# Kernel tuning notes

Measured on AMD Instinct MI355X. Metric: run time of the kernel, lower is better.

Reference implementation:

```python
import math
import jax, jax.numpy as jnp
import numpy as np

B, L, S, H, E, D = 2, 2048, 2048, 8, 64, 64


def setup_inputs() -> dict:
    key = jax.random.key(0)
    kq, kk, kv = jax.random.split(key, 3)
    return {
        "queries": jax.random.normal(kq, (B, L, H, E), dtype=jnp.float32),
        "keys": jax.random.normal(kk, (B, S, H, E), dtype=jnp.float32),
        "values": jax.random.normal(kv, (B, S, H, D), dtype=jnp.float32),
    }


def reference(queries, keys, values):
    b, l, h, e = queries.shape
    s = keys.shape[1]
    # source truncates queries if L > S
    if l > s:
        queries = queries[:, :s]
        l = s
    # dense scores [B,H,L,S]
    scores = jnp.einsum('blhe,bshe->bhls', queries, keys)
    # sparsity measure per query: max - mean over keys
    M_sp = scores.max(axis=-1) - scores.sum(axis=-1) / s  # [B,H,L]
    # k = min(max(L*log(S),1), L); for S>=3 this equals L (all queries, reordered)
    k = min(int(max(l * math.log(s), 1)), l)
    _, top_k = jax.lax.top_k(M_sp, k)  # [B,H,k], descending by M_sp
    # gather selected query rows of the score matrix
    topk_scores = jnp.take_along_axis(scores, top_k[..., None], axis=2)  # [B,H,k,S]
    topk_scores = topk_scores - topk_scores.max(axis=-1, keepdims=True)
    A = jax.nn.softmax(topk_scores / math.sqrt(e), axis=-1)  # [B,H,k,S]
    # attend (output in top-k-permuted query order, as in source)
    V = jnp.einsum('bhls,bshd->blhd', A, values)  # [B,k,H,D]
    return V
```

## Files before the change

### kernel.cpp

```cpp
#include <hip/hip_runtime.h>
#include <math.h>

#define BB 2
#define LL 2048
#define SS 2048
#define HH 8
#define EE 64
#define DD 64
#define HE (HH * EE)


typedef __attribute__((ext_vector_type(8))) short   bf16x8;
typedef __attribute__((ext_vector_type(4))) float   f32x4;
typedef __attribute__((ext_vector_type(8))) unsigned short u16x8;
typedef __attribute__((ext_vector_type(4))) unsigned short u16x4;

__device__ __forceinline__ unsigned short f2bf(float x) {
    unsigned int u = __float_as_uint(x);
    return (unsigned short)((u + 0x7FFFu + ((u >> 16) & 1u)) >> 16);
}

__device__ __forceinline__ float rdlane(float v, int lane) {
    return __uint_as_float(
        (unsigned)__builtin_amdgcn_readlane((int)__float_as_uint(v), lane));
}

__global__ __launch_bounds__(256, 2)
void msp_partial(const float* __restrict__ Q, const float* __restrict__ K,
                 float* __restrict__ pscratch) {
#pragma clang fp contract(off)
    const int bid = blockIdx.x;
    const int hf = bid >> 9;
    const int rem = bid & 511;
    const int lt = rem & 31, bh = rem >> 5;
    const int h = bh & 7, b = bh >> 3;
    const int t = threadIdx.x, lq = t & 63, w = t >> 6;
    const int l = lt * 64 + lq;

    float qf[64];
    const float4* qrow = (const float4*)(Q + (((size_t)b * LL + l) * HH + h) * EE);
#pragma unroll
    for (int i = 0; i < 16; i++) {
        float4 v = qrow[i];
        qf[4*i] = v.x; qf[4*i+1] = v.y; qf[4*i+2] = v.z; qf[4*i+3] = v.w;
    }

    const float* Kw = K + (((size_t)b * SS) * HH + h) * EE
                        + (size_t)(hf * 512 + w * 128) * HE;
    const float* gld = Kw + (size_t)(lq >> 4) * HE + (lq & 15) * 4;

    float4 A0 = *(const float4*)(gld);
    float4 B0 = *(const float4*)(gld + 4 * HE);

    float mx = -1e30f;
    float r[8];
#pragma unroll 1
    for (int i8 = 0; i8 < 16; ++i8) {
        const int kc = i8 * 8;
        const int kn = (kc < 120) ? kc + 8 : 120;

        float4 A1 = *(const float4*)(gld + (size_t)kn * HE);
        float4 B1 = *(const float4*)(gld + (size_t)(kn + 4) * HE);

        float c[8];
#pragma unroll
        for (int j = 0; j < 8; ++j) c[j] = 0.f;
#pragma unroll
        for (int j = 0; j < 4; ++j) {
#pragma unroll
            for (int e4 = 0; e4 < 16; ++e4) {
                const int ln = j * 16 + e4;
                c[j] = fmaf(qf[4*e4+0], rdlane(A0.x, ln), c[j]);
                c[j] = fmaf(qf[4*e4+1], rdlane(A0.y, ln), c[j]);
                c[j] = fmaf(qf[4*e4+2], rdlane(A0.z, ln), c[j]);
                c[j] = fmaf(qf[4*e4+3], rdlane(A0.w, ln), c[j]);
            }
        }
#pragma unroll
        for (int j = 0; j < 4; ++j) {
#pragma unroll
            for (int e4 = 0; e4 < 16; ++e4) {
                const int ln = j * 16 + e4;
                c[4+j] = fmaf(qf[4*e4+0], rdlane(B0.x, ln), c[4+j]);
                c[4+j] = fmaf(qf[4*e4+1], rdlane(B0.y, ln), c[4+j]);
                c[4+j] = fmaf(qf[4*e4+2], rdlane(B0.z, ln), c[4+j]);
                c[4+j] = fmaf(qf[4*e4+3], rdlane(B0.w, ln), c[4+j]);
            }
        }
#pragma unroll
        for (int j = 0; j < 8; ++j) {
            mx = fmaxf(mx, c[j]);
            if (i8 == 0) r[j] = c[j];
            else         r[j] = __fadd_rn(r[j], c[j]);
        }
        A0 = A1; B0 = B1;
    }
    const float blkv = __fadd_rn(
        __fadd_rn(__fadd_rn(r[0], r[1]), __fadd_rn(r[2], r[3])),
        __fadd_rn(__fadd_rn(r[4], r[5]), __fadd_rn(r[6], r[7])));

    __shared__ float smx[4][64], sblk[4][64];
    smx[w][lq] = mx; sblk[w][lq] = blkv;
    __syncthreads();
    if (w == 0) {
        const float m_all = fmaxf(fmaxf(smx[0][lq], smx[1][lq]),
                                  fmaxf(smx[2][lq], smx[3][lq]));
        const float sub = __fadd_rn(
            __fadd_rn(sblk[0][lq], sblk[1][lq]),
            __fadd_rn(sblk[2][lq], sblk[3][lq]));
        pscratch[(((size_t)hf * 16 + bh) << 11) + l]          = m_all;
        pscratch[131072 + (((size_t)hf * 16 + bh) << 11) + l] = sub;
    }
}

__global__ __launch_bounds__(1024)
void sort_rank(const float* __restrict__ pscratch, float* __restrict__ maxs,
               int* __restrict__ rank) {
    __shared__ unsigned int k1[2048];
    __shared__ int pay[2048];
    const int bh = blockIdx.x;
    const int t = threadIdx.x;
    for (int i = t; i < 2048; i += 1024) {
        const float p0 = pscratch[(((size_t)(0 * 16 + bh)) << 11) + i];
        const float p1 = pscratch[(((size_t)(1 * 16 + bh)) << 11) + i];
        const float p2 = pscratch[(((size_t)(2 * 16 + bh)) << 11) + i];
        const float p3 = pscratch[(((size_t)(3 * 16 + bh)) << 11) + i];
        const float s0 = pscratch[131072 + (((size_t)(0 * 16 + bh)) << 11) + i];
        const float s1 = pscratch[131072 + (((size_t)(1 * 16 + bh)) << 11) + i];
        const float s2 = pscratch[131072 + (((size_t)(2 * 16 + bh)) << 11) + i];
        const float s3 = pscratch[131072 + (((size_t)(3 * 16 + bh)) << 11) + i];
        const float m_all = fmaxf(fmaxf(p0, p1), fmaxf(p2, p3));
        const float s2048 = __fadd_rn(__fadd_rn(s0, s1), __fadd_rn(s2, s3));
        const float mean  = __fmul_rn(s2048, 0.00048828125f);
        const float msp   = __fsub_rn(m_all, mean);
        maxs[(((size_t)bh) << 11) + i] = m_all;
        unsigned int u = __float_as_uint(msp);
        u = (u & 0x80000000u) ? ~u : (u | 0x80000000u);
        k1[i] = u; pay[i] = i;
    }
    __syncthreads();
    for (int k = 2; k <= 2048; k <<= 1) {
        for (int j = k >> 1; j > 0; j >>= 1) {
            for (int i = t; i < 2048; i += 1024) {
                const int ixj = i ^ j;
                if (ixj > i) {
                    unsigned int a1 = k1[i], c1 = k1[ixj];
                    int pa = pay[i], pc = pay[ixj];
                    const bool pre = (a1 > c1) || (a1 == c1 && pa < pc);
                    const bool dir = ((i & k) == 0);
                    if (dir != pre) {
                        k1[i] = c1; k1[ixj] = a1;
                        pay[i] = pc; pay[ixj] = pa;
                    }
                }
            }
            __syncthreads();
        }
    }
    for (int i = t; i < 2048; i += 1024)
        rank[(((size_t)bh) << 11) + pay[i]] = i;
}

__global__ __launch_bounds__(256, 2)
void flash_mfma(const float* __restrict__ Q, const float* __restrict__ K,
                const float* __restrict__ V, const float* __restrict__ maxs,
                const int* __restrict__ rank, float* __restrict__ out) {
    __shared__ unsigned short ldsK[2][64 * 72];
    __shared__ unsigned short ldsVT[2][64 * 72];
    __shared__ unsigned short ldsP[4 * 16 * 72];

    const int bid = blockIdx.x;
    const int bh = bid & 15, lt = bid >> 4;
    const int h = bh & 7, b = bh >> 3;
    const int t = threadIdx.x, lane = t & 63, w = t >> 6;
    const int quad = lane >> 4, cl = lane & 15;

    const size_t kvbase = (((size_t)b * SS) * HH + h) * EE;

    bf16x8 qa[2];
    {
        const float* qp = Q + (((size_t)b * LL + (lt * 64 + w * 16 + cl)) * HH + h) * EE
                          + quad * 8;
#pragma unroll
        for (int ef = 0; ef < 2; ++ef) {
            float4 a0 = *(const float4*)(qp + ef * 32);
            float4 a1 = *(const float4*)(qp + ef * 32 + 4);
            short* s = (short*)&qa[ef];
            s[0] = (short)f2bf(a0.x); s[1] = (short)f2bf(a0.y);
            s[2] = (short)f2bf(a0.z); s[3] = (short)f2bf(a0.w);
            s[4] = (short)f2bf(a1.x); s[5] = (short)f2bf(a1.y);
            s[6] = (short)f2bf(a1.z); s[7] = (short)f2bf(a1.w);
        }
    }

    float negpm[4];
    int rk[4];
#pragma unroll
    for (int reg = 0; reg < 4; ++reg) {
        const int qg = lt * 64 + w * 16 + quad * 4 + reg;
        negpm[reg] = -0.125f * maxs[((size_t)bh << 11) + qg];
        rk[reg]    = rank[((size_t)bh << 11) + qg];
    }

    f32x4 accO[4];
#pragma unroll
    for (int nt = 0; nt < 4; ++nt) accO[nt] = (f32x4){0.f, 0.f, 0.f, 0.f};
    float ell[4] = {0.f, 0.f, 0.f, 0.f};

    const int pbase = w * (16 * 72);

    const int krow = t >> 2, kcol = (t & 3) * 16;
    const int vs0 = (t & 15) * 4, vd0 = (t >> 4) * 4;

    {
        const float* gp = K + kvbase + (size_t)krow * HE + kcol;
        float4 f0 = ((const float4*)gp)[0];
        float4 f1 = ((const float4*)gp)[1];
        float4 f2 = ((const float4*)gp)[2];
        float4 f3 = ((const float4*)gp)[3];
        const float* gv = V + kvbase + (size_t)vs0 * HE + vd0;
        float4 v0 = *(const float4*)(gv);
        float4 v1 = *(const float4*)(gv + HE);
        float4 v2 = *(const float4*)(gv + 2 * HE);
        float4 v3 = *(const float4*)(gv + 3 * HE);
        u16x8 w0 = { f2bf(f0.x), f2bf(f0.y), f2bf(f0.z), f2bf(f0.w),
                     f2bf(f1.x), f2bf(f1.y), f2bf(f1.z), f2bf(f1.w) };
        u16x8 w1 = { f2bf(f2.x), f2bf(f2.y), f2bf(f2.z), f2bf(f2.w),
                     f2bf(f3.x), f2bf(f3.y), f2bf(f3.z), f2bf(f3.w) };
        *(u16x8*)&ldsK[0][krow * 72 + kcol]     = w0;
        *(u16x8*)&ldsK[0][krow * 72 + kcol + 8] = w1;
        u16x4 p0 = { f2bf(v0.x), f2bf(v1.x), f2bf(v2.x), f2bf(v3.x) };
        u16x4 p1 = { f2bf(v0.y), f2bf(v1.y), f2bf(v2.y), f2bf(v3.y) };
        u16x4 p2 = { f2bf(v0.z), f2bf(v1.z), f2bf(v2.z), f2bf(v3.z) };
        u16x4 p3 = { f2bf(v0.w), f2bf(v1.w), f2bf(v2.w), f2bf(v3.w) };
        *(u16x4*)&ldsVT[0][(vd0 + 0) * 72 + vs0] = p0;
        *(u16x4*)&ldsVT[0][(vd0 + 1) * 72 + vs0] = p1;
        *(u16x4*)&ldsVT[0][(vd0 + 2) * 72 + vs0] = p2;
        *(u16x4*)&ldsVT[0][(vd0 + 3) * 72 + vs0] = p3;
    }
    __syncthreads();

    int cur = 0;
#pragma unroll 1
    for (int c0 = 0; c0 < SS; c0 += 64) {
        const bool more = (c0 + 64 < SS);
        float4 f0, f1, f2, f3, v0, v1, v2, v3;
        if (more) {
            const float* gp = K + kvbase + (size_t)(c0 + 64 + krow) * HE + kcol;
            f0 = ((const float4*)gp)[0];
            f1 = ((const float4*)gp)[1];
            f2 = ((const float4*)gp)[2];
            f3 = ((const float4*)gp)[3];
            const float* gv = V + kvbase + (size_t)(c0 + 64 + vs0) * HE + vd0;
            v0 = *(const float4*)(gv);
            v1 = *(const float4*)(gv + HE);
            v2 = *(const float4*)(gv + 2 * HE);
            v3 = *(const float4*)(gv + 3 * HE);
        }

        f32x4 Sc[4];
#pragma unroll
        for (int nt = 0; nt < 4; ++nt) {
            bf16x8 bk0 = *(const bf16x8*)&ldsK[cur][(nt * 16 + cl) * 72 + quad * 8];
            bf16x8 bk1 = *(const bf16x8*)&ldsK[cur][(nt * 16 + cl) * 72 + quad * 8 + 32];
            f32x4 z = (f32x4){0.f, 0.f, 0.f, 0.f};
            z = __builtin_amdgcn_mfma_f32_16x16x32_bf16(qa[0], bk0, z, 0, 0, 0);
            z = __builtin_amdgcn_mfma_f32_16x16x32_bf16(qa[1], bk1, z, 0, 0, 0);
            Sc[nt] = z;
        }

#pragma unroll
        for (int nt = 0; nt < 4; ++nt) {
#pragma unroll
            for (int reg = 0; reg < 4; ++reg) {
                const float p = __expf(fmaf(Sc[nt][reg], 0.125f, negpm[reg]));
                ell[reg] += p;
                ldsP[pbase + (quad * 4 + reg) * 72 + nt * 16 + cl] = f2bf(p);
            }
        }

        bf16x8 pa0 = *(const bf16x8*)&ldsP[pbase + cl * 72 + quad * 8];
        bf16x8 pa1 = *(const bf16x8*)&ldsP[pbase + cl * 72 + quad * 8 + 32];
#pragma unroll
        for (int nt = 0; nt < 4; ++nt) {
            bf16x8 bv0 = *(const bf16x8*)&ldsVT[cur][(nt * 16 + cl) * 72 + quad * 8];
            bf16x8 bv1 = *(const bf16x8*)&ldsVT[cur][(nt * 16 + cl) * 72 + quad * 8 + 32];
            accO[nt] = __builtin_amdgcn_mfma_f32_16x16x32_bf16(pa0, bv0, accO[nt], 0, 0, 0);
            accO[nt] = __builtin_amdgcn_mfma_f32_16x16x32_bf16(pa1, bv1, accO[nt], 0, 0, 0);
        }

        if (more) {
            u16x8 w0 = { f2bf(f0.x), f2bf(f0.y), f2bf(f0.z), f2bf(f0.w),
                         f2bf(f1.x), f2bf(f1.y), f2bf(f1.z), f2bf(f1.w) };
            u16x8 w1 = { f2bf(f2.x), f2bf(f2.y), f2bf(f2.z), f2bf(f2.w),
                         f2bf(f3.x), f2bf(f3.y), f2bf(f3.z), f2bf(f3.w) };
            *(u16x8*)&ldsK[cur ^ 1][krow * 72 + kcol]     = w0;
            *(u16x8*)&ldsK[cur ^ 1][krow * 72 + kcol + 8] = w1;
            u16x4 p0 = { f2bf(v0.x), f2bf(v1.x), f2bf(v2.x), f2bf(v3.x) };
            u16x4 p1 = { f2bf(v0.y), f2bf(v1.y), f2bf(v2.y), f2bf(v3.y) };
            u16x4 p2 = { f2bf(v0.z), f2bf(v1.z), f2bf(v2.z), f2bf(v3.z) };
            u16x4 p3 = { f2bf(v0.w), f2bf(v1.w), f2bf(v2.w), f2bf(v3.w) };
            *(u16x4*)&ldsVT[cur ^ 1][(vd0 + 0) * 72 + vs0] = p0;
            *(u16x4*)&ldsVT[cur ^ 1][(vd0 + 1) * 72 + vs0] = p1;
            *(u16x4*)&ldsVT[cur ^ 1][(vd0 + 2) * 72 + vs0] = p2;
            *(u16x4*)&ldsVT[cur ^ 1][(vd0 + 3) * 72 + vs0] = p3;
        }
        __syncthreads();
        cur ^= 1;
    }

#pragma unroll
    for (int reg = 0; reg < 4; ++reg) {
        float e = ell[reg];
        e += __shfl_xor(e, 1);
        e += __shfl_xor(e, 2);
        e += __shfl_xor(e, 4);
        e += __shfl_xor(e, 8);
        ell[reg] = 1.0f / e;
    }

#pragma unroll
    for (int reg = 0; reg < 4; ++reg) {
        float* orow = out + (((size_t)b * LL + rk[reg]) * HH + h) * DD;
#pragma unroll
        for (int nt = 0; nt < 4; ++nt)
            orow[nt * 16 + cl] = accO[nt][reg] * ell[reg];
    }
}

extern "C" void kernel_launch(void* const* d_in, const int* in_sizes, int n_in,
                              void* d_out, int out_size, void* d_ws, size_t ws_size,
                              hipStream_t stream) {
    const float* Q = (const float*)d_in[0];
    const float* K = (const float*)d_in[1];
    const float* V = (const float*)d_in[2];
    float* out = (float*)d_out;

    int*   rank = (int*)((char*)d_ws + 131072);
    float* maxs = (float*)((char*)d_ws + 262144);

    msp_partial<<<4 * BB * HH * (LL / 64), 256, 0, stream>>>(Q, K, out);
    sort_rank<<<BB * HH, 1024, 0, stream>>>(out, maxs, rank);
    flash_mfma<<<BB * HH * (LL / 64), 256, 0, stream>>>(Q, K, V, maxs, rank, out);
}
```

Measured before the change: 354.1 us.

## Give each wave private 16-key K/V tiles to drop block barriers

Each wave now loads and converts its own 16-key slice of K and V into private LDS buffers and walks the key dimension 16 at a time, which removes the block-wide __syncthreads from the main loop. The aim is to cut barrier stalls between waves. In exchange every wave re-reads all of K and V from global memory, four times the block's previous traffic. The PV MFMA now runs half-empty because lanes in quads 2-3 feed zeros, and the single-buffered tiles leave little room to hide load latency.

```diff
diff --git a/kernel.cpp b/kernel.cpp
--- a/kernel.cpp
+++ b/kernel.cpp
@@ -165,15 +165,16 @@
 void flash_mfma(const float* __restrict__ Q, const float* __restrict__ K,
                 const float* __restrict__ V, const float* __restrict__ maxs,
                 const int* __restrict__ rank, float* __restrict__ out) {
-    __shared__ unsigned short ldsK[2][64 * 72];
-    __shared__ unsigned short ldsVT[2][64 * 72];
-    __shared__ unsigned short ldsP[4 * 16 * 72];
+    __shared__ unsigned short ldsK[4][16 * 72];
+    __shared__ unsigned short ldsVT[4][64 * 24];
+    __shared__ unsigned short ldsP[4][16 * 72];
 
     const int bid = blockIdx.x;
     const int bh = bid & 15, lt = bid >> 4;
     const int h = bh & 7, b = bh >> 3;
     const int t = threadIdx.x, lane = t & 63, w = t >> 6;
     const int quad = lane >> 4, cl = lane & 15;
+    const int qq = quad & 1;
 
     const size_t kvbase = (((size_t)b * SS) * HH + h) * EE;
 
@@ -207,106 +208,93 @@
     for (int nt = 0; nt < 4; ++nt) accO[nt] = (f32x4){0.f, 0.f, 0.f, 0.f};
     float ell[4] = {0.f, 0.f, 0.f, 0.f};
 
-    const int pbase = w * (16 * 72);
-
-    const int krow = t >> 2, kcol = (t & 3) * 16;
-    const int vs0 = (t & 15) * 4, vd0 = (t >> 4) * 4;
+    unsigned short* Kw  = ldsK[w];
+    unsigned short* VTw = ldsVT[w];
+    unsigned short* Pw  = ldsP[w];
+
+    const int kr = lane >> 2, kc = (lane & 3) * 16;
+    const int vd = (lane >> 2) * 4, vs = (lane & 3) * 4;
+
+    float4 kf0, kf1, kf2, kf3, vf0, vf1, vf2, vf3;
 
     {
-        const float* gp = K + kvbase + (size_t)krow * HE + kcol;
-        float4 f0 = ((const float4*)gp)[0];
-        float4 f1 = ((const float4*)gp)[1];
-        float4 f2 = ((const float4*)gp)[2];
-        float4 f3 = ((const float4*)gp)[3];
-        const float* gv = V + kvbase + (size_t)vs0 * HE + vd0;
-        float4 v0 = *(const float4*)(gv);
-        float4 v1 = *(const float4*)(gv + HE);
-        float4 v2 = *(const float4*)(gv + 2 * HE);
-        float4 v3 = *(const float4*)(gv + 3 * HE);
-        u16x8 w0 = { f2bf(f0.x), f2bf(f0.y), f2bf(f0.z), f2bf(f0.w),
-                     f2bf(f1.x), f2bf(f1.y), f2bf(f1.z), f2bf(f1.w) };
-        u16x8 w1 = { f2bf(f2.x), f2bf(f2.y), f2bf(f2.z), f2bf(f2.w),
-                     f2bf(f3.x), f2bf(f3.y), f2bf(f3.z), f2bf(f3.w) };
-        *(u16x8*)&ldsK[0][krow * 72 + kcol]     = w0;
-        *(u16x8*)&ldsK[0][krow * 72 + kcol + 8] = w1;
-        u16x4 p0 = { f2bf(v0.x), f2bf(v1.x), f2bf(v2.x), f2bf(v3.x) };
-        u16x4 p1 = { f2bf(v0.y), f2bf(v1.y), f2bf(v2.y), f2bf(v3.y) };
-        u16x4 p2 = { f2bf(v0.z), f2bf(v1.z), f2bf(v2.z), f2bf(v3.z) };
-        u16x4 p3 = { f2bf(v0.w), f2bf(v1.w), f2bf(v2.w), f2bf(v3.w) };
-        *(u16x4*)&ldsVT[0][(vd0 + 0) * 72 + vs0] = p0;
-        *(u16x4*)&ldsVT[0][(vd0 + 1) * 72 + vs0] = p1;
-        *(u16x4*)&ldsVT[0][(vd0 + 2) * 72 + vs0] = p2;
-        *(u16x4*)&ldsVT[0][(vd0 + 3) * 72 + vs0] = p3;
-    }
-    __syncthreads();
-
-    int cur = 0;
+        const float* gp = K + kvbase + (size_t)kr * HE + kc;
+        kf0 = ((const float4*)gp)[0]; kf1 = ((const float4*)gp)[1];
+        kf2 = ((const float4*)gp)[2]; kf3 = ((const float4*)gp)[3];
+        const float* gv = V + kvbase + (size_t)vs * HE + vd;
+        vf0 = *(const float4*)(gv);
+        vf1 = *(const float4*)(gv + HE);
+        vf2 = *(const float4*)(gv + 2 * HE);
+        vf3 = *(const float4*)(gv + 3 * HE);
+        u16x8 a = { f2bf(kf0.x), f2bf(kf0.y), f2bf(kf0.z), f2bf(kf0.w),
+                    f2bf(kf1.x), f2bf(kf1.y), f2bf(kf1.z), f2bf(kf1.w) };
+        u16x8 b2 = { f2bf(kf2.x), f2bf(kf2.y), f2bf(kf2.z), f2bf(kf2.w),
+                     f2bf(kf3.x), f2bf(kf3.y), f2bf(kf3.z), f2bf(kf3.w) };
+        *(u16x8*)&Kw[kr * 72 + kc]     = a;
+        *(u16x8*)&Kw[kr * 72 + kc + 8] = b2;
+        u16x4 p0 = { f2bf(vf0.x), f2bf(vf1.x), f2bf(vf2.x), f2bf(vf3.x) };
+        u16x4 p1 = { f2bf(vf0.y), f2bf(vf1.y), f2bf(vf2.y), f2bf(vf3.y) };
+        u16x4 p2 = { f2bf(vf0.z), f2bf(vf1.z), f2bf(vf2.z), f2bf(vf3.z) };
+        u16x4 p3 = { f2bf(vf0.w), f2bf(vf1.w), f2bf(vf2.w), f2bf(vf3.w) };
+        *(u16x4*)&VTw[(vd + 0) * 24 + vs] = p0;
+        *(u16x4*)&VTw[(vd + 1) * 24 + vs] = p1;
+        *(u16x4*)&VTw[(vd + 2) * 24 + vs] = p2;
+        *(u16x4*)&VTw[(vd + 3) * 24 + vs] = p3;
+    }
+
+    const bf16x8 zero8 = (bf16x8){0, 0, 0, 0, 0, 0, 0, 0};
+
 #pragma unroll 1
-    for (int c0 = 0; c0 < SS; c0 += 64) {
-        const bool more = (c0 + 64 < SS);
-        float4 f0, f1, f2, f3, v0, v1, v2, v3;
+    for (int c0 = 0; c0 < SS; c0 += 16) {
+        const bool more = (c0 + 16 < SS);
         if (more) {
-            const float* gp = K + kvbase + (size_t)(c0 + 64 + krow) * HE + kcol;
-            f0 = ((const float4*)gp)[0];
-            f1 = ((const float4*)gp)[1];
-            f2 = ((const float4*)gp)[2];
-            f3 = ((const float4*)gp)[3];
-            const float* gv = V + kvbase + (size_t)(c0 + 64 + vs0) * HE + vd0;
-            v0 = *(const float4*)(gv);
-            v1 = *(const float4*)(gv + HE);
-            v2 = *(const float4*)(gv + 2 * HE);
-            v3 = *(const float4*)(gv + 3 * HE);
-        }
-
-        f32x4 Sc[4];
+            const float* gp = K + kvbase + (size_t)(c0 + 16 + kr) * HE + kc;
+            kf0 = ((const float4*)gp)[0]; kf1 = ((const float4*)gp)[1];
+            kf2 = ((const float4*)gp)[2]; kf3 = ((const float4*)gp)[3];
+            const float* gv = V + kvbase + (size_t)(c0 + 16 + vs) * HE + vd;
+            vf0 = *(const float4*)(gv);
+            vf1 = *(const float4*)(gv + HE);
+            vf2 = *(const float4*)(gv + 2 * HE);
+            vf3 = *(const float4*)(gv + 3 * HE);
+        }
+
+        bf16x8 bk0 = *(const bf16x8*)&Kw[cl * 72 + quad * 8];
+        bf16x8 bk1 = *(const bf16x8*)&Kw[cl * 72 + quad * 8 + 32];
+        f32x4 z = (f32x4){0.f, 0.f, 0.f, 0.f};
+        z = __builtin_amdgcn_mfma_f32_16x16x32_bf16(qa[0], bk0, z, 0, 0, 0);
+        z = __builtin_amdgcn_mfma_f32_16x16x32_bf16(qa[1], bk1, z, 0, 0, 0);
+
+#pragma unroll
+        for (int reg = 0; reg < 4; ++reg) {
+            const float p = __expf(fmaf(z[reg], 0.125f, negpm[reg]));
+            ell[reg] += p;
+            Pw[(quad * 4 + reg) * 72 + cl] = f2bf(p);
+        }
+
+        bf16x8 par = *(const bf16x8*)&Pw[cl * 72 + qq * 8];
+        bf16x8 pa = (quad < 2) ? par : zero8;
 #pragma unroll
         for (int nt = 0; nt < 4; ++nt) {
-            bf16x8 bk0 = *(const bf16x8*)&ldsK[cur][(nt * 16 + cl) * 72 + quad * 8];
-            bf16x8 bk1 = *(const bf16x8*)&ldsK[cur][(nt * 16 + cl) * 72 + quad * 8 + 32];
-            f32x4 z = (f32x4){0.f, 0.f, 0.f, 0.f};
-            z = __builtin_amdgcn_mfma_f32_16x16x32_bf16(qa[0], bk0, z, 0, 0, 0);
-            z = __builtin_amdgcn_mfma_f32_16x16x32_bf16(qa[1], bk1, z, 0, 0, 0);
-            Sc[nt] = z;
-        }
-
-#pragma unroll
-        for (int nt = 0; nt < 4; ++nt) {
-#pragma unroll
-            for (int reg = 0; reg < 4; ++reg) {
-                const float p = __expf(fmaf(Sc[nt][reg], 0.125f, negpm[reg]));
-                ell[reg] += p;
-                ldsP[pbase + (quad * 4 + reg) * 72 + nt * 16 + cl] = f2bf(p);
-            }
-        }
-
-        bf16x8 pa0 = *(const bf16x8*)&ldsP[pbase + cl * 72 + quad * 8];
-        bf16x8 pa1 = *(const bf16x8*)&ldsP[pbase + cl * 72 + quad * 8 + 32];
-#pragma unroll
-        for (int nt = 0; nt < 4; ++nt) {
-            bf16x8 bv0 = *(const bf16x8*)&ldsVT[cur][(nt * 16 + cl) * 72 + quad * 8];
-            bf16x8 bv1 = *(const bf16x8*)&ldsVT[cur][(nt * 16 + cl) * 72 + quad * 8 + 32];
-            accO[nt] = __builtin_amdgcn_mfma_f32_16x16x32_bf16(pa0, bv0, accO[nt], 0, 0, 0);
-            accO[nt] = __builtin_amdgcn_mfma_f32_16x16x32_bf16(pa1, bv1, accO[nt], 0, 0, 0);
+            bf16x8 bv = *(const bf16x8*)&VTw[(nt * 16 + cl) * 24 + qq * 8];
+            accO[nt] = __builtin_amdgcn_mfma_f32_16x16x32_bf16(pa, bv, accO[nt], 0, 0, 0);
         }
 
         if (more) {
-            u16x8 w0 = { f2bf(f0.x), f2bf(f0.y), f2bf(f0.z), f2bf(f0.w),
-                         f2bf(f1.x), f2bf(f1.y), f2bf(f1.z), f2bf(f1.w) };
-            u16x8 w1 = { f2bf(f2.x), f2bf(f2.y), f2bf(f2.z), f2bf(f2.w),
-                         f2bf(f3.x), f2bf(f3.y), f2bf(f3.z), f2bf(f3.w) };
-            *(u16x8*)&ldsK[cur ^ 1][krow * 72 + kcol]     = w0;
-            *(u16x8*)&ldsK[cur ^ 1][krow * 72 + kcol + 8] = w1;
-            u16x4 p0 = { f2bf(v0.x), f2bf(v1.x), f2bf(v2.x), f2bf(v3.x) };
-            u16x4 p1 = { f2bf(v0.y), f2bf(v1.y), f2bf(v2.y), f2bf(v3.y) };
-            u16x4 p2 = { f2bf(v0.z), f2bf(v1.z), f2bf(v2.z), f2bf(v3.z) };
-            u16x4 p3 = { f2bf(v0.w), f2bf(v1.w), f2bf(v2.w), f2bf(v3.w) };
-            *(u16x4*)&ldsVT[cur ^ 1][(vd0 + 0) * 72 + vs0] = p0;
-            *(u16x4*)&ldsVT[cur ^ 1][(vd0 + 1) * 72 + vs0] = p1;
-            *(u16x4*)&ldsVT[cur ^ 1][(vd0 + 2) * 72 + vs0] = p2;
-            *(u16x4*)&ldsVT[cur ^ 1][(vd0 + 3) * 72 + vs0] = p3;
-        }
-        __syncthreads();
-        cur ^= 1;
+            u16x8 a = { f2bf(kf0.x), f2bf(kf0.y), f2bf(kf0.z), f2bf(kf0.w),
+                        f2bf(kf1.x), f2bf(kf1.y), f2bf(kf1.z), f2bf(kf1.w) };
+            u16x8 b2 = { f2bf(kf2.x), f2bf(kf2.y), f2bf(kf2.z), f2bf(kf2.w),
+                         f2bf(kf3.x), f2bf(kf3.y), f2bf(kf3.z), f2bf(kf3.w) };
+            *(u16x8*)&Kw[kr * 72 + kc]     = a;
+            *(u16x8*)&Kw[kr * 72 + kc + 8] = b2;
+            u16x4 p0 = { f2bf(vf0.x), f2bf(vf1.x), f2bf(vf2.x), f2bf(vf3.x) };
+            u16x4 p1 = { f2bf(vf0.y), f2bf(vf1.y), f2bf(vf2.y), f2bf(vf3.y) };
+            u16x4 p2 = { f2bf(vf0.z), f2bf(vf1.z), f2bf(vf2.z), f2bf(vf3.z) };
+            u16x4 p3 = { f2bf(vf0.w), f2bf(vf1.w), f2bf(vf2.w), f2bf(vf3.w) };
+            *(u16x4*)&VTw[(vd + 0) * 24 + vs] = p0;
+            *(u16x4*)&VTw[(vd + 1) * 24 + vs] = p1;
+            *(u16x4*)&VTw[(vd + 2) * 24 + vs] = p2;
+            *(u16x4*)&VTw[(vd + 3) * 24 + vs] = p3;
+        }
     }
 
 #pragma unroll
```

New measurement: 464.7 us. 1.31x slower.
